# Optimization experiments

Hardware: AMD Instinct MI355X
Metric: run time of the kernel (lower is better)

The kernel has to match this reference:

```python
import jax, jax.numpy as jnp
import numpy as np

N_PATCHES = 14
HIDDEN_D = 768
N_HEADS = 12
D_HEAD = HIDDEN_D // N_HEADS
OUT_D = 1000
IMG = 224
C = 3
PS = IMG // N_PATCHES  # 16
SEQ = N_PATCHES * N_PATCHES + 1  # 197
INPUT_D = C * PS * PS  # 768
EPS = 1e-5


def positional_embeddings(s, d):
    i = jnp.arange(s, dtype=jnp.float32)[:, None]
    j = jnp.arange(d, dtype=jnp.float32)[None, :]
    even = jnp.sin(i / jnp.power(10000.0, j / d))
    odd = jnp.cos(i / jnp.power(10000.0, (j - 1.0) / d))
    return jnp.where(jnp.arange(d)[None, :] % 2 == 0, even, odd)


def layernorm_2d(x, g, b):
    # torch nn.LayerNorm((S, D)): normalize over last two dims jointly, biased var
    mu = jnp.mean(x, axis=(-2, -1), keepdims=True)
    var = jnp.var(x, axis=(-2, -1), keepdims=True)
    return (x - mu) * jax.lax.rsqrt(var + EPS) * g + b


def setup_inputs() -> dict:
    key = jax.random.key(0)
    ks = jax.random.split(key, 16)
    s = 0.02
    return {
        "images": jax.random.normal(ks[0], (64, C, IMG, IMG), jnp.float32),
        "W_map": jax.random.normal(ks[1], (INPUT_D, HIDDEN_D), jnp.float32) * s,
        "b_map": jnp.zeros((HIDDEN_D,), jnp.float32),
        "cls_tok": jax.random.uniform(ks[2], (1, HIDDEN_D), jnp.float32),
        "ln1_g": jnp.ones((SEQ, HIDDEN_D), jnp.float32),
        "ln1_b": jnp.zeros((SEQ, HIDDEN_D), jnp.float32),
        "Wq": jax.random.normal(ks[3], (N_HEADS, D_HEAD, D_HEAD), jnp.float32) * s,
        "bq": jnp.zeros((N_HEADS, D_HEAD), jnp.float32),
        "Wk": jax.random.normal(ks[4], (N_HEADS, D_HEAD, D_HEAD), jnp.float32) * s,
        "bk": jnp.zeros((N_HEADS, D_HEAD), jnp.float32),
        "Wv": jax.random.normal(ks[5], (N_HEADS, D_HEAD, D_HEAD), jnp.float32) * s,
        "bv": jnp.zeros((N_HEADS, D_HEAD), jnp.float32),
        "ln2_g": jnp.ones((SEQ, HIDDEN_D), jnp.float32),
        "ln2_b": jnp.zeros((SEQ, HIDDEN_D), jnp.float32),
        "W_enc": jax.random.normal(ks[6], (HIDDEN_D, HIDDEN_D), jnp.float32) * s,
        "b_enc": jnp.zeros((HIDDEN_D,), jnp.float32),
        "W_out": jax.random.normal(ks[7], (HIDDEN_D, OUT_D), jnp.float32) * s,
        "b_out": jnp.zeros((OUT_D,), jnp.float32),
    }


def reference(images, W_map, b_map, cls_tok, ln1_g, ln1_b, Wq, bq, Wk, bk, Wv, bv,
              ln2_g, ln2_b, W_enc, b_enc, W_out, b_out):
    n = images.shape[0]
    # patchify: [N,C,H,W] -> [N, np*np, C*ps*ps], patch flattened in (C,ph,pw) order
    p = images.reshape(n, C, N_PATCHES, PS, N_PATCHES, PS)
    patches = p.transpose(0, 2, 4, 1, 3, 5).reshape(n, N_PATCHES * N_PATCHES, INPUT_D)

    tokens = patches @ W_map + b_map  # [N, np^2, D]
    cls = jnp.broadcast_to(cls_tok[None], (n, 1, HIDDEN_D))
    tokens = jnp.concatenate([cls, tokens], axis=1)  # [N, S, D]
    tokens = tokens + positional_embeddings(SEQ, HIDDEN_D)[None]

    # MSA on ln1(tokens), vectorized over batch and heads
    x = layernorm_2d(tokens, ln1_g, ln1_b)
    xh = x.reshape(n, SEQ, N_HEADS, D_HEAD)  # split hidden into heads
    q = jnp.einsum('bshd,hde->bshe', xh, Wq) + bq[None, None]
    k = jnp.einsum('bshd,hde->bshe', xh, Wk) + bk[None, None]
    v = jnp.einsum('bshd,hde->bshe', xh, Wv) + bv[None, None]
    scores = jnp.einsum('bshe,bthe->bhst', q, k) / np.sqrt(D_HEAD).astype(np.float32)
    attn = jax.nn.softmax(scores, axis=-1)  # [B,H,S,S]
    msa = jnp.einsum('bhst,bthe->bshe', attn, v).reshape(n, SEQ, HIDDEN_D)

    out = tokens + msa
    out = out + jax.nn.relu(layernorm_2d(out, ln2_g, ln2_b) @ W_enc + b_enc)
    cls_out = out[:, 0]  # [N, D]
    return jax.nn.softmax(cls_out @ W_out + b_out, axis=-1)
```

## Files before the change

kernel.cpp:

```cpp
#include <hip/hip_runtime.h>
#include <math.h>

#define SEQL 197
#define HD 768
#define NH 12
#define DHD 64
#define BATCH 64
#define OUTD 1000

typedef unsigned short ushort_t;
typedef __attribute__((ext_vector_type(8))) short bf16x8;
typedef __attribute__((ext_vector_type(4))) float f32x4;

static __device__ __forceinline__ unsigned short f2bf(float f) {
    union { float f; unsigned u; } v; v.f = f;
    unsigned r = v.u + 0x7fff + ((v.u >> 16) & 1);
    return (unsigned short)(r >> 16);
}

static __device__ __forceinline__ void gload16(const ushort_t* g, ushort_t* l) {
    __builtin_amdgcn_global_load_lds(
        (const __attribute__((address_space(1))) unsigned int*)g,
        (__attribute__((address_space(3))) unsigned int*)l, 16, 0, 0);
}

static __device__ __forceinline__ int xcd_chunk(int id, int nwg) {
    int xcd = id & 7, ii = id >> 3;
    int q = nwg >> 3, r = nwg & 7;
    return (xcd < r) ? (xcd * (q + 1) + ii) : (r * (q + 1) + (xcd - r) * q + ii);
}

#define NB_CVT  1296
#define NB_INIT 783
__global__ void k_prep(const float* __restrict__ W_map, const float* __restrict__ W_enc,
                       const float* __restrict__ Wq, const float* __restrict__ Wk,
                       const float* __restrict__ Wv, const float* __restrict__ cls_tok,
                       const float* __restrict__ img,
                       ushort_t* __restrict__ WmT, ushort_t* __restrict__ WeT,
                       ushort_t* __restrict__ wt, float* __restrict__ stats,
                       float* __restrict__ logits, float* __restrict__ pos,
                       float* __restrict__ tok, ushort_t* __restrict__ Ae) {
    const int bx = blockIdx.x, tid = threadIdx.x;
    if (bx < NB_CVT) {
        int idx = bx * 256 + tid;
        if (bx == 0) { stats[tid] = 0.f; }
        if (idx < BATCH * OUTD) logits[idx] = 0.f;
        if (idx < 2 * 147456) {
            const float* W = (idx < 147456) ? W_map : W_enc;
            ushort_t* WT   = (idx < 147456) ? WmT : WeT;
            int i = (idx < 147456) ? idx : idx - 147456;
            int k = i / 192, nq = i % 192;
            float4 w = *(const float4*)&W[k * 768 + nq * 4];
            WT[(nq * 4 + 0) * 768 + k] = f2bf(w.x);
            WT[(nq * 4 + 1) * 768 + k] = f2bf(w.y);
            WT[(nq * 4 + 2) * 768 + k] = f2bf(w.z);
            WT[(nq * 4 + 3) * 768 + k] = f2bf(w.w);
        } else {
            int i = idx - 2 * 147456;
            if (i < 36864) {
                int dq = i & 15;
                int e  = (i >> 4) & 63;
                int h  = (i >> 10) % 12;
                int pj = i / 12288;
                const float* W = (pj == 0) ? Wq : (pj == 1) ? Wk : Wv;
                ushort4 o;
                o.x = f2bf(W[(h * 64 + dq * 4 + 0) * 64 + e]);
                o.y = f2bf(W[(h * 64 + dq * 4 + 1) * 64 + e]);
                o.z = f2bf(W[(h * 64 + dq * 4 + 2) * 64 + e]);
                o.w = f2bf(W[(h * 64 + dq * 4 + 3) * 64 + e]);
                *(ushort4*)&wt[(size_t)((pj * 12 + h) * 64 + e) * 64 + dq * 4] = o;
            }
        }
    } else if (bx < NB_CVT + NB_INIT) {
        int i = (bx - NB_CVT) * 256 + tid;
        if (i < SEQL * HD) {
            int s = i / HD, d = i % HD;
            float f = (float)(d & ~1);
            float r = powf(10000.0f, -f / (float)HD);
            float a = (float)s * r;
            pos[i] = (d & 1) ? cosf(a) : sinf(a);
        } else {
            int j = i - SEQL * HD;
            int b = j / HD, e = j % HD;
            tok[(b * SEQL) * HD + e] = cls_tok[e] + ((e & 1) ? 1.0f : 0.0f);
        }
    } else if (bx == NB_CVT + NB_INIT) {
        __shared__ float rs[4], rs2[4];
        float s = 0.f, s2 = 0.f;
#pragma unroll
        for (int j = 0; j < 3; ++j) {
            int e = tid * 3 + j;
            float v = cls_tok[e] + ((e & 1) ? 1.0f : 0.0f);
            s += v; s2 += v * v;
        }
#pragma unroll
        for (int off = 32; off > 0; off >>= 1) {
            s += __shfl_down(s, off);
            s2 += __shfl_down(s2, off);
        }
        int lane = tid & 63, w = tid >> 6;
        if (lane == 0) { rs[w] = s; rs2[w] = s2; }
        __syncthreads();
        if (tid == 0) {
            float S = 0.f, S2 = 0.f;
#pragma unroll
            for (int i = 0; i < 4; ++i) { S += rs[i]; S2 += rs2[i]; }
            stats[256] = S;
            stats[257] = S2;
        }
    } else {
        int idx = (bx - (NB_CVT + NB_INIT + 1)) * 256 + tid;
        int m = idx / 192, kq = idx % 192;
        int k0 = kq * 4;
        int c = k0 >> 8, rem = k0 & 255, ir = rem >> 4, jc = rem & 15;
        int b = m / 196, pi = m % 196;
        int pr = pi / 14, pc = pi % 14;
        float4 v = *(const float4*)&img[((b * 3 + c) * 224 + pr * 16 + ir) * 224 + pc * 16 + jc];
        ushort4 o;
        o.x = f2bf(v.x); o.y = f2bf(v.y); o.z = f2bf(v.z); o.w = f2bf(v.w);
        *(ushort4*)&Ae[m * 768 + k0] = o;
    }
}

template <int MODE>
__launch_bounds__(256)
__global__ void k_gemm_bf16(const ushort_t* __restrict__ A, const ushort_t* __restrict__ Bt,
                            const float* __restrict__ bias, const float* __restrict__ pos,
                            float* __restrict__ out, int Mtot, float* __restrict__ stats,
                            int nwg) {
    __shared__ ushort_t As[128 * 64];
    __shared__ ushort_t Bs[128 * 64];
    __shared__ float redS[4][4];
    const int vid = xcd_chunk(blockIdx.x, nwg);
    const int m0 = (vid / 6) * 128;
    const int n0 = (vid % 6) * 128;
    const int tid = threadIdx.x;
    const int lane = tid & 63, wave = tid >> 6;
    const int wm = wave >> 1, wn = wave & 1;

    f32x4 acc[4][4];
#pragma unroll
    for (int i = 0; i < 4; ++i)
#pragma unroll
        for (int j = 0; j < 4; ++j)
#pragma unroll
            for (int r = 0; r < 4; ++r) acc[i][j][r] = 0.f;

    for (int kt = 0; kt < 12; ++kt) {
        const int k0 = kt * 64;
#pragma unroll
        for (int t = 0; t < 4; ++t) {
            int c = (wave << 2) | t;
            int o = c * 1024 + lane * 16;
            int row = o >> 7;
            int inner = o & 127;
            int col = (inner ^ ((row & 7) << 4)) >> 1;
            gload16(&A[(size_t)(m0 + row) * 768 + k0 + col], &As[c * 512]);
            gload16(&Bt[(size_t)(n0 + row) * 768 + k0 + col], &Bs[c * 512]);
        }
        __syncthreads();
#pragma unroll
        for (int ks = 0; ks < 2; ++ks) {
            const int cbyte = ks * 64 + (lane >> 4) * 16;
            bf16x8 af[4], bf[4];
#pragma unroll
            for (int mi = 0; mi < 4; ++mi) {
                int row = wm * 64 + mi * 16 + (lane & 15);
                af[mi] = *(const bf16x8*)((const char*)As + row * 128 + (cbyte ^ ((row & 7) << 4)));
            }
#pragma unroll
            for (int ni = 0; ni < 4; ++ni) {
                int n = wn * 64 + ni * 16 + (lane & 15);
                bf[ni] = *(const bf16x8*)((const char*)Bs + n * 128 + (cbyte ^ ((n & 7) << 4)));
            }
#pragma unroll
            for (int mi = 0; mi < 4; ++mi)
#pragma unroll
                for (int ni = 0; ni < 4; ++ni)
                    acc[mi][ni] = __builtin_amdgcn_mfma_f32_16x16x32_bf16(af[mi], bf[ni], acc[mi][ni], 0, 0, 0);
        }
        __syncthreads();
    }

    const int colb = n0 + wn * 64 + (lane & 15);
    const int rowb = m0 + wm * 64 + (lane >> 4) * 4;
    float s_lo = 0.f, q_lo = 0.f, s_hi = 0.f, q_hi = 0.f;
    const int bA = m0 / 196;
    const int mSplit = (bA + 1) * 196;
#pragma unroll
    for (int ni = 0; ni < 4; ++ni) {
        const int n = colb + ni * 16;
        const float bn = bias[n];
#pragma unroll
        for (int mi = 0; mi < 4; ++mi) {
#pragma unroll
            for (int r = 0; r < 4; ++r) {
                int m = rowb + mi * 16 + r;
                if (MODE == 0) {
                    int b = m / 196, s = 1 + m % 196;
                    float oval = acc[mi][ni][r] + bn + pos[s * HD + n];
                    out[((b * SEQL) + s) * HD + n] = oval;
                    if (m < mSplit) { s_lo += oval; q_lo += oval * oval; }
                    else            { s_hi += oval; q_hi += oval * oval; }
                } else {
                    if (m < Mtot) {
                        float* p = &out[(size_t)m * HD + n];
                        *p = *p + fmaxf(acc[mi][ni][r] + bn, 0.f);
                    }
                }
            }
        }
    }
    if (MODE == 0) {
#pragma unroll
        for (int off = 32; off > 0; off >>= 1) {
            s_lo += __shfl_down(s_lo, off);
            q_lo += __shfl_down(q_lo, off);
            s_hi += __shfl_down(s_hi, off);
            q_hi += __shfl_down(q_hi, off);
        }
        if (lane == 0) {
            redS[wave][0] = s_lo; redS[wave][1] = q_lo;
            redS[wave][2] = s_hi; redS[wave][3] = q_hi;
        }
        __syncthreads();
        if (tid == 0) {
            float a0 = 0.f, a1 = 0.f, a2 = 0.f, a3 = 0.f;
#pragma unroll
            for (int i = 0; i < 4; ++i) {
                a0 += redS[i][0]; a1 += redS[i][1];
                a2 += redS[i][2]; a3 += redS[i][3];
            }
            atomicAdd(&stats[2 * bA], a0);
            atomicAdd(&stats[2 * bA + 1], a1);
            int bB = bA + 1;
            if (bB < BATCH) {
                atomicAdd(&stats[2 * bB], a2);
                atomicAdd(&stats[2 * bB + 1], a3);
            }
        }
    }
}

__launch_bounds__(512, 2)
__global__ void k_qkvattn(const float* __restrict__ tok, float* __restrict__ stats,
                          const float* __restrict__ g1, const float* __restrict__ b1,
                          const ushort_t* __restrict__ wt,
                          const float* __restrict__ bq, const float* __restrict__ bk,
                          const float* __restrict__ bv, float* __restrict__ out) {
    const int h = blockIdx.x, b = blockIdx.y;
    __shared__ __attribute__((aligned(16))) ushort_t sm[32768];
    __shared__ float rS[8], rS2[8];
    const int tid = threadIdx.x;
    const int wave = tid >> 6, lane = tid & 63;
    const int l16 = lane & 15, l4 = lane >> 4;
    const int r0 = wave * 32;
    const float inv_n = 1.0f / (float)(SEQL * HD);
    const float S1_ = stats[b * 2] + stats[256];
    const float S2_ = stats[b * 2 + 1] + stats[257];
    const float mu = S1_ * inv_n;
    const float rsg = rsqrtf(S2_ * inv_n - mu * mu + 1e-5f);
    ushort_t* A16 = sm;
    ushort_t* B16 = sm + 16384;

    {
        const int row = tid >> 1, hw = tid & 1;
        if (row < SEQL) {
            const float* tp = &tok[((size_t)b * SEQL + row) * HD + h * 64 + hw * 32];
            const float* gp = &g1[(size_t)row * HD + h * 64 + hw * 32];
            const float* bp = &b1[(size_t)row * HD + h * 64 + hw * 32];
#pragma unroll
            for (int g = 0; g < 4; ++g) {
                float4 t0 = *(const float4*)&tp[g * 8];
                float4 t1 = *(const float4*)&tp[g * 8 + 4];
                float4 ga = *(const float4*)&gp[g * 8];
                float4 gb = *(const float4*)&gp[g * 8 + 4];
                float4 ba = *(const float4*)&bp[g * 8];
                float4 bb = *(const float4*)&bp[g * 8 + 4];
                bf16x8 o;
                o[0] = (short)f2bf((t0.x - mu) * rsg * ga.x + ba.x);
                o[1] = (short)f2bf((t0.y - mu) * rsg * ga.y + ba.y);
                o[2] = (short)f2bf((t0.z - mu) * rsg * ga.z + ba.z);
                o[3] = (short)f2bf((t0.w - mu) * rsg * ga.w + ba.w);
                o[4] = (short)f2bf((t1.x - mu) * rsg * gb.x + bb.x);
                o[5] = (short)f2bf((t1.y - mu) * rsg * gb.y + bb.y);
                o[6] = (short)f2bf((t1.z - mu) * rsg * gb.z + bb.z);
                o[7] = (short)f2bf((t1.w - mu) * rsg * gb.w + bb.w);
                int pc = (hw * 32 + g * 8) ^ ((row & 7) << 3);
                *(bf16x8*)&A16[row * 64 + pc] = o;
            }
        } else {
            bf16x8 z;
#pragma unroll
            for (int j = 0; j < 8; ++j) z[j] = 0;
#pragma unroll
            for (int g = 0; g < 4; ++g) {
                int pc = (hw * 32 + g * 8) ^ ((row & 7) << 3);
                *(bf16x8*)&A16[row * 64 + pc] = z;
            }
        }
    }

    bf16x8 af[2][2];
#pragma unroll
    for (int mi = 0; mi < 2; ++mi)
#pragma unroll
        for (int kk = 0; kk < 2; ++kk) {
            int row = r0 + mi * 16 + l16;
            af[mi][kk] = *(const bf16x8*)&A16[row * 64 + ((kk * 32 + l4 * 8) ^ ((row & 7) << 3))];
        }

#define PROJ_ACC(PJ, ACC)                                                                      \
    {                                                                                          \
        _Pragma("unroll") for (int ni = 0; ni < 4; ++ni) {                                     \
            const ushort_t* wr = &wt[(size_t)(((PJ) * 12 + h) * 64 + ni * 16 + l16) * 64];     \
            bf16x8 w0 = *(const bf16x8*)&wr[l4 * 8];                                           \
            bf16x8 w1 = *(const bf16x8*)&wr[32 + l4 * 8];                                      \
            _Pragma("unroll") for (int mi = 0; mi < 2; ++mi) {                                 \
                ACC[mi][ni] = __builtin_amdgcn_mfma_f32_16x16x32_bf16(af[mi][0], w0, ACC[mi][ni], 0, 0, 0); \
                ACC[mi][ni] = __builtin_amdgcn_mfma_f32_16x16x32_bf16(af[mi][1], w1, ACC[mi][ni], 0, 0, 0); \
            }                                                                                  \
        }                                                                                      \
    }

    f32x4 acc[2][4];
#define ZERO_ACC                                                                               \
    _Pragma("unroll") for (int mi = 0; mi < 2; ++mi)                                           \
        _Pragma("unroll") for (int ni = 0; ni < 4; ++ni) {                                     \
            acc[mi][ni][0] = 0.f; acc[mi][ni][1] = 0.f; acc[mi][ni][2] = 0.f; acc[mi][ni][3] = 0.f; }

    ZERO_ACC;
    PROJ_ACC(0, acc);
#pragma unroll
    for (int ni = 0; ni < 4; ++ni) {
        float bn = bq[h * 64 + ni * 16 + l16];
#pragma unroll
        for (int mi = 0; mi < 2; ++mi)
#pragma unroll
            for (int r = 0; r < 4; ++r) {
                int row = r0 + mi * 16 + l4 * 4 + r;
                A16[row * 64 + ((ni * 16 + l16) ^ ((row & 7) << 3))] = f2bf(acc[mi][ni][r] + bn);
            }
    }
    bf16x8 qa[2][2];
#pragma unroll
    for (int mi = 0; mi < 2; ++mi)
#pragma unroll
        for (int kk = 0; kk < 2; ++kk) {
            int row = r0 + mi * 16 + l16;
            qa[mi][kk] = *(const bf16x8*)&A16[row * 64 + ((kk * 32 + l4 * 8) ^ ((row & 7) << 3))];
        }

    ZERO_ACC;
    PROJ_ACC(1, acc);
#pragma unroll
    for (int ni = 0; ni < 4; ++ni) {
        float bn = bk[h * 64 + ni * 16 + l16];
#pragma unroll
        for (int mi = 0; mi < 2; ++mi)
#pragma unroll
            for (int r = 0; r < 4; ++r) {
                int t = r0 + mi * 16 + l4 * 4 + r;
                A16[t * 64 + ((ni * 16 + l16) ^ ((t & 7) << 3))] = f2bf(acc[mi][ni][r] + bn);
            }
    }

    ZERO_ACC;
    PROJ_ACC(2, acc);
#pragma unroll
    for (int ni = 0; ni < 4; ++ni) {
        float bn = bv[h * 64 + ni * 16 + l16];
#pragma unroll
        for (int mi = 0; mi < 2; ++mi) {
            int t4 = r0 + mi * 16 + l4 * 4;
            int e = ni * 16 + l16;
            ushort4 pkt;
            pkt.x = f2bf(acc[mi][ni][0] + bn);
            pkt.y = f2bf(acc[mi][ni][1] + bn);
            pkt.z = f2bf(acc[mi][ni][2] + bn);
            pkt.w = f2bf(acc[mi][ni][3] + bn);
            *(ushort4*)&B16[e * 256 + (t4 ^ ((e & 7) << 3))] = pkt;
        }
    }

    __syncthreads();

    f32x4 sa[2][16];
#pragma unroll
    for (int ni = 0; ni < 16; ++ni) {
        int t = ni * 16 + l16;
        bf16x8 k0 = *(const bf16x8*)&A16[t * 64 + ((l4 * 8) ^ ((t & 7) << 3))];
        bf16x8 k1 = *(const bf16x8*)&A16[t * 64 + ((32 + l4 * 8) ^ ((t & 7) << 3))];
#pragma unroll
        for (int mi = 0; mi < 2; ++mi) {
            f32x4 z;
            z[0] = 0.f; z[1] = 0.f; z[2] = 0.f; z[3] = 0.f;
            z = __builtin_amdgcn_mfma_f32_16x16x32_bf16(qa[mi][0], k0, z, 0, 0, 0);
            sa[mi][ni] = __builtin_amdgcn_mfma_f32_16x16x32_bf16(qa[mi][1], k1, z, 0, 0, 0);
        }
    }

    float l_s[2][4];
#pragma unroll
    for (int mi = 0; mi < 2; ++mi)
#pragma unroll
        for (int r = 0; r < 4; ++r) {
            float rsum = 0.f;
#pragma unroll
            for (int ni = 0; ni < 16; ++ni) {
                float p = (ni * 16 + l16 < SEQL) ? __expf(sa[mi][ni][r] * 0.125f) : 0.f;
                sa[mi][ni][r] = p;
                rsum += p;
            }
            rsum += __shfl_xor(rsum, 1);
            rsum += __shfl_xor(rsum, 2);
            rsum += __shfl_xor(rsum, 4);
            rsum += __shfl_xor(rsum, 8);
            l_s[mi][r] = rsum;
        }

    __syncthreads();

    f32x4 oacc[2][4];
#pragma unroll
    for (int mi = 0; mi < 2; ++mi)
#pragma unroll
        for (int ne = 0; ne < 4; ++ne) {
            oacc[mi][ne][0] = 0.f; oacc[mi][ne][1] = 0.f;
            oacc[mi][ne][2] = 0.f; oacc[mi][ne][3] = 0.f;
        }

    for (int c = 0; c < 4; ++c) {
#pragma unroll
        for (int j = 0; j < 4; ++j)
#pragma unroll
            for (int mi = 0; mi < 2; ++mi)
#pragma unroll
                for (int r = 0; r < 4; ++r) {
                    int row = r0 + mi * 16 + l4 * 4 + r;
                    A16[row * 64 + ((j * 16 + l16) ^ ((row & 7) << 3))] = f2bf(sa[mi][c * 4 + j][r]);
                }
        bf16x8 pa[2][2];
#pragma unroll
        for (int mi = 0; mi < 2; ++mi)
#pragma unroll
            for (int kk = 0; kk < 2; ++kk) {
                int row = r0 + mi * 16 + l16;
                pa[mi][kk] = *(const bf16x8*)&A16[row * 64 + ((kk * 32 + l4 * 8) ^ ((row & 7) << 3))];
            }
#pragma unroll
        for (int ne = 0; ne < 4; ++ne) {
            int e = ne * 16 + l16;
            bf16x8 v0 = *(const bf16x8*)&B16[e * 256 + ((c * 64 + l4 * 8) ^ ((e & 7) << 3))];
            bf16x8 v1 = *(const bf16x8*)&B16[e * 256 + ((c * 64 + 32 + l4 * 8) ^ ((e & 7) << 3))];
#pragma unroll
            for (int mi = 0; mi < 2; ++mi) {
                oacc[mi][ne] = __builtin_amdgcn_mfma_f32_16x16x32_bf16(pa[mi][0], v0, oacc[mi][ne], 0, 0, 0);
                oacc[mi][ne] = __builtin_amdgcn_mfma_f32_16x16x32_bf16(pa[mi][1], v1, oacc[mi][ne], 0, 0, 0);
            }
        }
    }

    __syncthreads();
    float* Osm = (float*)sm + wave * 2048;
#pragma unroll
    for (int mi = 0; mi < 2; ++mi)
#pragma unroll
        for (int r = 0; r < 4; ++r) {
            float inv = 1.0f / l_s[mi][r];
            int rl = mi * 16 + l4 * 4 + r;
#pragma unroll
            for (int ne = 0; ne < 4; ++ne)
                Osm[rl * 64 + ((ne * 16 + l16) ^ ((rl & 3) << 4))] = oacc[mi][ne][r] * inv;
        }
    float psum = 0.f, psq = 0.f;
#pragma unroll
    for (int it = 0; it < 8; ++it) {
        int rl = it * 4 + l4;
        int row = r0 + rl;
        if (row < SEQL) {
            size_t off = ((size_t)b * SEQL + row) * HD + h * 64 + l16 * 4;
            float4 ov = *(float4*)&Osm[rl * 64 + ((l16 * 4) ^ ((rl & 3) << 4))];
            float4 tv = *(const float4*)&tok[off];
            float4 o;
            o.x = ov.x + tv.x; o.y = ov.y + tv.y;
            o.z = ov.z + tv.z; o.w = ov.w + tv.w;
            *(float4*)&out[off] = o;
            psum += o.x + o.y + o.z + o.w;
            psq  += o.x * o.x + o.y * o.y + o.z * o.z + o.w * o.w;
        }
    }
#pragma unroll
    for (int off = 32; off > 0; off >>= 1) {
        psum += __shfl_down(psum, off);
        psq += __shfl_down(psq, off);
    }
    if (lane == 0) { rS[wave] = psum; rS2[wave] = psq; }
    __syncthreads();
    if (tid == 0) {
        float S = 0.f, S2 = 0.f;
#pragma unroll
        for (int i = 0; i < 8; ++i) { S += rS[i]; S2 += rS2[i]; }
        atomicAdd(&stats[128 + 2 * b], S);
        atomicAdd(&stats[129 + 2 * b], S2);
    }
#undef PROJ_ACC
#undef ZERO_ACC
}

__global__ void k_ln2apply(const float* __restrict__ outb, const float* __restrict__ stats,
                           const float* __restrict__ g2, const float* __restrict__ b2,
                           ushort_t* __restrict__ x) {
    int i = blockIdx.x * 256 + threadIdx.x;
    if (i >= BATCH * SEQL * HD / 4) return;
    int e4 = i * 4;
    int m = e4 / HD, kk = e4 % HD;
    int b = m / SEQL, s = m % SEQL;
    const float inv_n = 1.0f / (float)(SEQL * HD);
    float S = stats[128 + 2 * b], S2 = stats[129 + 2 * b];
    float mu = S * inv_n;
    float rsg = rsqrtf(S2 * inv_n - mu * mu + 1e-5f);
    float4 t = *(const float4*)&outb[e4];
    float4 g = *(const float4*)&g2[s * HD + kk];
    float4 bb = *(const float4*)&b2[s * HD + kk];
    ushort4 o;
    o.x = f2bf((t.x - mu) * rsg * g.x + bb.x);
    o.y = f2bf((t.y - mu) * rsg * g.y + bb.y);
    o.z = f2bf((t.z - mu) * rsg * g.z + bb.z);
    o.w = f2bf((t.w - mu) * rsg * g.w + bb.w);
    *(ushort4*)&x[e4] = o;
}

__launch_bounds__(256)
__global__ void k_logits(const float* __restrict__ out, const float* __restrict__ Wo,
                         float* __restrict__ logits) {
    const int eg = blockIdx.x, b = blockIdx.y, tid = threadIdx.x;
    __shared__ float cls[192];
    if (tid < 48)
        *(float4*)&cls[tid * 4] = *(const float4*)&out[(size_t)(b * SEQL) * HD + eg * 192 + tid * 4];
    __syncthreads();
    const int o0 = tid * 4;
    if (o0 < OUTD) {
        float4 acc = {0.f, 0.f, 0.f, 0.f};
        const float* wbase = &Wo[(size_t)eg * 192 * OUTD + o0];
#pragma unroll 4
        for (int e = 0; e < 192; ++e) {
            float c = cls[e];
            float4 w = *(const float4*)&wbase[(size_t)e * OUTD];
            acc.x += c * w.x;
            acc.y += c * w.y;
            acc.z += c * w.z;
            acc.w += c * w.w;
        }
        atomicAdd(&logits[b * OUTD + o0 + 0], acc.x);
        atomicAdd(&logits[b * OUTD + o0 + 1], acc.y);
        atomicAdd(&logits[b * OUTD + o0 + 2], acc.z);
        atomicAdd(&logits[b * OUTD + o0 + 3], acc.w);
    }
}

__launch_bounds__(256)
__global__ void k_head_sm(const float* __restrict__ logits, const float* __restrict__ bo,
                          float* __restrict__ dout) {
    const int b = blockIdx.x, tid = threadIdx.x;
    __shared__ float red[256];
    const int o0 = tid * 4;
    const bool ok = (o0 < OUTD);
    float4 acc = {0.f, 0.f, 0.f, 0.f};
    if (ok) {
        float4 lg = *(const float4*)&logits[b * OUTD + o0];
        float4 bb = *(const float4*)&bo[o0];
        acc.x = lg.x + bb.x; acc.y = lg.y + bb.y;
        acc.z = lg.z + bb.z; acc.w = lg.w + bb.w;
    }
    float mx = ok ? fmaxf(fmaxf(acc.x, acc.y), fmaxf(acc.z, acc.w)) : -INFINITY;
    red[tid] = mx;
    __syncthreads();
    for (int s = 128; s > 0; s >>= 1) {
        if (tid < s) red[tid] = fmaxf(red[tid], red[tid + s]);
        __syncthreads();
    }
    float M = red[0];
    __syncthreads();
    float4 p = {0.f, 0.f, 0.f, 0.f};
    float ls = 0.f;
    if (ok) {
        p.x = expf(acc.x - M);
        p.y = expf(acc.y - M);
        p.z = expf(acc.z - M);
        p.w = expf(acc.w - M);
        ls = p.x + p.y + p.z + p.w;
    }
    red[tid] = ls;
    __syncthreads();
    for (int s = 128; s > 0; s >>= 1) {
        if (tid < s) red[tid] += red[tid + s];
        __syncthreads();
    }
    float inv = 1.0f / red[0];
    if (ok) {
        p.x *= inv; p.y *= inv; p.z *= inv; p.w *= inv;
        *(float4*)&dout[b * OUTD + o0] = p;
    }
}

extern "C" void kernel_launch(void* const* d_in, const int* in_sizes, int n_in,
                              void* d_out, int out_size, void* d_ws, size_t ws_size,
                              hipStream_t stream) {
    const float* images  = (const float*)d_in[0];
    const float* W_map   = (const float*)d_in[1];
    const float* b_map   = (const float*)d_in[2];
    const float* cls_tok = (const float*)d_in[3];
    const float* ln1_g   = (const float*)d_in[4];
    const float* ln1_b   = (const float*)d_in[5];
    const float* Wq      = (const float*)d_in[6];
    const float* bq      = (const float*)d_in[7];
    const float* Wk      = (const float*)d_in[8];
    const float* bk      = (const float*)d_in[9];
    const float* Wv      = (const float*)d_in[10];
    const float* bv      = (const float*)d_in[11];
    const float* ln2_g   = (const float*)d_in[12];
    const float* ln2_b   = (const float*)d_in[13];
    const float* W_enc   = (const float*)d_in[14];
    const float* b_enc   = (const float*)d_in[15];
    const float* W_out   = (const float*)d_in[16];
    const float* b_out   = (const float*)d_in[17];

    float* ws = (float*)d_ws;
    const size_t BIG = (size_t)BATCH * SEQL * HD;

    float* pos   = ws;
    float* tok   = ws + 151552;
    float* outb  = tok + BIG;
    float* stats = outb + BIG;
    ushort_t* wtq = (ushort_t*)(stats + 512);
    ushort_t* Ae  = wtq + 147456;
    ushort_t* WmT = Ae + (size_t)12672 * 768;
    ushort_t* WeT = WmT + (size_t)768 * 768;
    float* logits = (float*)(WeT + (size_t)768 * 768);
    ushort_t* Ae2 = Ae;

    k_prep<<<11488, 256, 0, stream>>>(W_map, W_enc, Wq, Wk, Wv, cls_tok, images,
                                      WmT, WeT, wtq, stats, logits, pos, tok, Ae);
    k_gemm_bf16<0><<<588, 256, 0, stream>>>(Ae, WmT, b_map, pos, tok, 12544, stats, 588);
    k_qkvattn<<<dim3(12, 64), 512, 0, stream>>>(tok, stats, ln1_g, ln1_b, wtq, bq, bk, bv, outb);
    k_ln2apply<<<9456, 256, 0, stream>>>(outb, stats, ln2_g, ln2_b, Ae2);
    k_gemm_bf16<1><<<594, 256, 0, stream>>>(Ae2, WeT, b_enc, pos, outb, 12608, stats, 594);
    k_logits<<<dim3(4, 64), 256, 0, stream>>>(outb, W_out, logits);
    k_head_sm<<<64, 256, 0, stream>>>(logits, b_out, (float*)d_out);
}
```

Baseline: 233.8 us.

## Double-buffer LDS tiles in bf16 GEMM to overlap global loads with MFMA

The GEMM's A and B shared-memory tiles are now double-buffered. The async global-to-LDS loads for the next K tile are issued before the MFMA work on the current tile, with one barrier per iteration instead of two. This is meant to hide global memory latency behind compute. It doubles LDS use to about 64KB per block, which may reduce occupancy. The correctness of reading the next buffer depends on the vmcnt wait that the barrier implies.

```diff
diff --git a/kernel.cpp b/kernel.cpp
--- a/kernel.cpp
+++ b/kernel.cpp
@@ -128,8 +128,8 @@
                             const float* __restrict__ bias, const float* __restrict__ pos,
                             float* __restrict__ out, int Mtot, float* __restrict__ stats,
                             int nwg) {
-    __shared__ ushort_t As[128 * 64];
-    __shared__ ushort_t Bs[128 * 64];
+    __shared__ ushort_t As[2][128 * 64];
+    __shared__ ushort_t Bs[2][128 * 64];
     __shared__ float redS[4][4];
     const int vid = xcd_chunk(blockIdx.x, nwg);
     const int m0 = (vid / 6) * 128;
@@ -138,6 +138,28 @@
     const int lane = tid & 63, wave = tid >> 6;
     const int wm = wave >> 1, wn = wave & 1;
 
+    int stg_c[4], stg_row[4], stg_col[4];
+#pragma unroll
+    for (int t = 0; t < 4; ++t) {
+        int c = (wave << 2) | t;
+        int o = c * 1024 + lane * 16;
+        int row = o >> 7;
+        int inner = o & 127;
+        stg_c[t] = c;
+        stg_row[t] = row;
+        stg_col[t] = (inner ^ ((row & 7) << 4)) >> 1;
+    }
+
+#define STAGE(BUF, K0)                                                                    \
+    {                                                                                     \
+        _Pragma("unroll") for (int t = 0; t < 4; ++t) {                                   \
+            gload16(&A[(size_t)(m0 + stg_row[t]) * 768 + (K0) + stg_col[t]],              \
+                    &As[BUF][stg_c[t] * 512]);                                            \
+            gload16(&Bt[(size_t)(n0 + stg_row[t]) * 768 + (K0) + stg_col[t]],             \
+                    &Bs[BUF][stg_c[t] * 512]);                                            \
+        }                                                                                 \
+    }
+
     f32x4 acc[4][4];
 #pragma unroll
     for (int i = 0; i < 4; ++i)
@@ -146,19 +168,13 @@
 #pragma unroll
             for (int r = 0; r < 4; ++r) acc[i][j][r] = 0.f;
 
+    STAGE(0, 0);
+    __syncthreads();
+
+    int cur = 0;
     for (int kt = 0; kt < 12; ++kt) {
-        const int k0 = kt * 64;
-#pragma unroll
-        for (int t = 0; t < 4; ++t) {
-            int c = (wave << 2) | t;
-            int o = c * 1024 + lane * 16;
-            int row = o >> 7;
-            int inner = o & 127;
-            int col = (inner ^ ((row & 7) << 4)) >> 1;
-            gload16(&A[(size_t)(m0 + row) * 768 + k0 + col], &As[c * 512]);
-            gload16(&Bt[(size_t)(n0 + row) * 768 + k0 + col], &Bs[c * 512]);
-        }
-        __syncthreads();
+        if (kt < 11) STAGE(cur ^ 1, (kt + 1) * 64);
+
 #pragma unroll
         for (int ks = 0; ks < 2; ++ks) {
             const int cbyte = ks * 64 + (lane >> 4) * 16;
@@ -166,12 +182,12 @@
 #pragma unroll
             for (int mi = 0; mi < 4; ++mi) {
                 int row = wm * 64 + mi * 16 + (lane & 15);
-                af[mi] = *(const bf16x8*)((const char*)As + row * 128 + (cbyte ^ ((row & 7) << 4)));
+                af[mi] = *(const bf16x8*)((const char*)&As[cur][0] + row * 128 + (cbyte ^ ((row & 7) << 4)));
             }
 #pragma unroll
             for (int ni = 0; ni < 4; ++ni) {
                 int n = wn * 64 + ni * 16 + (lane & 15);
-                bf[ni] = *(const bf16x8*)((const char*)Bs + n * 128 + (cbyte ^ ((n & 7) << 4)));
+                bf[ni] = *(const bf16x8*)((const char*)&Bs[cur][0] + n * 128 + (cbyte ^ ((n & 7) << 4)));
             }
 #pragma unroll
             for (int mi = 0; mi < 4; ++mi)
@@ -180,7 +196,9 @@
                     acc[mi][ni] = __builtin_amdgcn_mfma_f32_16x16x32_bf16(af[mi], bf[ni], acc[mi][ni], 0, 0, 0);
         }
         __syncthreads();
-    }
+        cur ^= 1;
+    }
+#undef STAGE
 
     const int colb = n0 + wn * 64 + (lane & 15);
     const int rowb = m0 + wm * 64 + (lane >> 4) * 4;
```

New measurement: 233.5 us, median of 2. Within noise of the previous version (-0.2%).
